# Optimization experiments

Hardware: AMD Instinct MI355X
Metric: run time of the kernel (lower is better)

The kernel has to match this reference:

```python
import jax, jax.numpy as jnp
import numpy as np

MAX_CACHE_LEN = 4096


def _rotate_half(t):
    d = t.shape[-1] // 2
    return jnp.concatenate([-t[..., d:], t[..., :d]], axis=-1)


def _apply_rope(t, cos, sin):
    # t: (B, S, H, D); cos/sin: (S, D)
    c = cos[None, :, None, :]
    s = sin[None, :, None, :]
    return t * c + _rotate_half(t) * s


def setup_inputs() -> dict:
    key = jax.random.key(0)
    ks = jax.random.split(key, 7)
    B, S, E, D, KVH = 1, 2048, 2048, 64, 8
    sc = 0.02
    x = jax.random.normal(ks[0], (B, S, E), dtype=jnp.float32)
    Wq = jax.random.normal(ks[1], (E, E), dtype=jnp.float32) * sc
    Wk = jax.random.normal(ks[2], (KVH * D, E), dtype=jnp.float32) * sc
    Wv = jax.random.normal(ks[3], (KVH * D, E), dtype=jnp.float32) * sc
    Wo = jax.random.normal(ks[4], (E, E), dtype=jnp.float32) * sc
    # RoPE tables
    pos = jnp.arange(S, dtype=jnp.float32)[:, None]
    inv_freq = 1.0 / (10000.0 ** (jnp.arange(0, D, 2, dtype=jnp.float32) / D))
    ang = pos * inv_freq[None, :]              # (S, D/2)
    ang = jnp.concatenate([ang, ang], axis=-1)  # (S, D)
    cos = jnp.cos(ang)
    sin = jnp.sin(ang)
    # additive causal mask (1,1,S,S): 0 where allowed, -1e9 where masked
    causal = jnp.tril(jnp.ones((S, S), dtype=bool))
    attn_mask = jnp.where(causal, 0.0, -1e9).astype(jnp.float32)[None, None]
    return {"x": x, "Wq": Wq, "Wk": Wk, "Wv": Wv, "Wo": Wo,
            "cos": cos, "sin": sin, "attn_mask": attn_mask, "last_pos": S}


def reference(x, Wq, Wk, Wv, Wo, cos, sin, attn_mask, last_pos):
    B, S, E = x.shape
    D = cos.shape[-1]
    H = E // D
    KVH = Wk.shape[0] // D
    group = H // KVH

    q = (x @ Wq.T).reshape(B, S, H, D)
    k = (x @ Wk.T).reshape(B, S, KVH, D)
    v = (x @ Wv.T).reshape(B, S, KVH, D)

    q = _apply_rope(q, cos, sin)
    k = _apply_rope(k, cos, sin)

    # KV-cache write (index_copy at positions [last_pos-S, last_pos)), then slice [:last_pos]
    key_cache = jnp.zeros((B, MAX_CACHE_LEN, KVH, D), dtype=x.dtype)
    value_cache = jnp.zeros((B, MAX_CACHE_LEN, KVH, D), dtype=x.dtype)
    key_cache = jax.lax.dynamic_update_slice(key_cache, jax.lax.stop_gradient(k), (0, last_pos - S, 0, 0))
    value_cache = jax.lax.dynamic_update_slice(value_cache, jax.lax.stop_gradient(v), (0, last_pos - S, 0, 0))
    kc = key_cache[:, :last_pos]    # (B, T, KVH, D)
    vc = value_cache[:, :last_pos]

    # GQA: repeat kv heads to match q heads
    kc = jnp.repeat(kc, group, axis=2)  # (B, T, H, D)
    vc = jnp.repeat(vc, group, axis=2)

    scale = 1.0 / np.sqrt(D)
    scores = jnp.einsum('bqhd,bkhd->bhqk', q, kc) * scale
    scores = scores + attn_mask
    probs = jax.nn.softmax(scores.astype(jnp.float32), axis=-1).astype(x.dtype)
    attn = jnp.einsum('bhqk,bkhd->bqhd', probs, vc)  # (B, S, H, D)
    out = attn.reshape(B, S, E) @ Wo.T
    return out
```

## Files before the change

kernel.cpp:

```cpp
#include <hip/hip_runtime.h>
#include <stdint.h>

typedef unsigned short u16;
typedef unsigned int   u32;

typedef __bf16 bf16x8 __attribute__((ext_vector_type(8)));
typedef float  fx4    __attribute__((ext_vector_type(4)));
typedef u16    u16x8  __attribute__((ext_vector_type(8)));
typedef u16    u16x4  __attribute__((ext_vector_type(4)));

typedef __attribute__((address_space(1))) unsigned int as1_u32;
typedef __attribute__((address_space(3))) unsigned int as3_u32;

__device__ __forceinline__ void gload_lds16(const void* g, void* lds) {
  __builtin_amdgcn_global_load_lds((const as1_u32*)(uintptr_t)g,
                                   (as3_u32*)(uintptr_t)lds, 16, 0, 0);
}

__device__ __forceinline__ float b2f(u32 bits) {
  union { u32 i; float f; } v; v.i = bits << 16; return v.f;
}
__device__ __forceinline__ u16 f2b(float f) {
  union { float f; u32 i; } v; v.f = f;
  u32 x = v.i;
  return (u16)((x + 0x7fffu + ((x >> 16) & 1u)) >> 16);
}
__device__ __forceinline__ u16 f2b_hw(float f) {
  union { __bf16 b; u16 u; } v; v.b = (__bf16)f; return v.u;
}
__device__ __forceinline__ float exp2_hw(float f) {
  return __builtin_amdgcn_exp2f(f);
}

__global__ __launch_bounds__(256) void cast_kernel(
    const float* __restrict__ s0, const float* __restrict__ s1,
    const float* __restrict__ s2, const float* __restrict__ s3,
    const float* __restrict__ s4, u16* __restrict__ dst)
{
  const size_t i8 = ((size_t)blockIdx.x * 256 + threadIdx.x) * 8;
  if (i8 >= 14680064) return;
  const float* src; size_t off;
  if      (i8 <  4194304) { src = s0; off = i8; }
  else if (i8 <  8388608) { src = s1; off = i8 - 4194304; }
  else if (i8 <  9437184) { src = s2; off = i8 - 8388608; }
  else if (i8 < 10485760) { src = s3; off = i8 - 9437184; }
  else                    { src = s4; off = i8 - 10485760; }
  const float4 a = *(const float4*)(src + off);
  const float4 b = *(const float4*)(src + off + 4);
  u16x8 o;
  o[0] = f2b(a.x); o[1] = f2b(a.y); o[2] = f2b(a.z); o[3] = f2b(a.w);
  o[4] = f2b(b.x); o[5] = f2b(b.y); o[6] = f2b(b.z); o[7] = f2b(b.w);
  *(u16x8*)(dst + i8) = o;
}

template <int MODE>
__global__ __launch_bounds__(512) void gemm_bt(
    const u16* __restrict__ A, const u16* __restrict__ B0,
    const u16* __restrict__ B1, const u16* __restrict__ B2,
    void* __restrict__ Cv, int K, int split1, int split2, int ldc,
    const float* __restrict__ cosb, const float* __restrict__ sinb,
    u16* __restrict__ vtg)
{
  __shared__ __align__(16) u16 smem[5 * 8192];

  const int n0 = blockIdx.x * 128;
  const int m0 = blockIdx.y * 128;

  const u16* Bsel; int nb;
  if (n0 < split1)      { Bsel = B0; nb = n0; }
  else if (n0 < split2) { Bsel = B1; nb = n0 - split1; }
  else                  { Bsel = B2; nb = n0 - split2; }

  const int tid  = threadIdx.x;
  const int wave = tid >> 6, lane = tid & 63;
  const int wm = wave >> 1, wn = wave & 1;
  const int quad = lane >> 4, l16 = lane & 15;

  fx4 acc[2][4];
#pragma unroll
  for (int i = 0; i < 2; ++i)
#pragma unroll
    for (int j = 0; j < 4; ++j) acc[i][j] = fx4{0.f, 0.f, 0.f, 0.f};

  const int row = tid >> 2;
  const int ch  = tid & 3;
  const int csw = (ch ^ ((row >> 1) & 3)) * 8;
  auto stage = [&](int kt, int buf) {
    u16* As = smem + buf * 8192;
    u16* Bs = As + 4096;
    const int k0 = kt * 32;
    gload_lds16(A    + (size_t)(m0 + row) * K + k0 + csw, As + tid * 8);
    gload_lds16(Bsel + (size_t)(nb + row) * K + k0 + csw, Bs + tid * 8);
  };

  const int KT = K >> 5;
  stage(0, 0); stage(1, 1); stage(2, 2); stage(3, 3);
  int bufR = 0, bufW = 4;

  const int fx = (l16 >> 1) & 3;
  const int cA = (quad ^ fx) * 8;

#pragma unroll 1
  for (int kt = 0; kt < KT; ++kt) {
    const int rem = KT - 1 - kt;
    if (rem >= 3)      asm volatile("s_waitcnt vmcnt(6)\n\ts_barrier" ::: "memory");
    else if (rem == 2) asm volatile("s_waitcnt vmcnt(4)\n\ts_barrier" ::: "memory");
    else if (rem == 1) asm volatile("s_waitcnt vmcnt(2)\n\ts_barrier" ::: "memory");
    else               asm volatile("s_waitcnt vmcnt(0)\n\ts_barrier" ::: "memory");
    if (kt + 4 < KT) stage(kt + 4, bufW);

    const u16* As = smem + bufR * 8192;
    const u16* Bs = As + 4096;

    bf16x8 af[2], bfr[4];
#pragma unroll
    for (int t = 0; t < 2; ++t)
      af[t]  = *(const bf16x8*)&As[(wm * 32 + t * 16 + l16) * 32 + cA];
#pragma unroll
    for (int t = 0; t < 4; ++t)
      bfr[t] = *(const bf16x8*)&Bs[(wn * 64 + t * 16 + l16) * 32 + cA];
#pragma unroll
    for (int ti = 0; ti < 2; ++ti)
#pragma unroll
      for (int tj = 0; tj < 4; ++tj)
        acc[ti][tj] = __builtin_amdgcn_mfma_f32_16x16x32_bf16(
            af[ti], bfr[tj], acc[ti][tj], 0, 0, 0);

    bufR = (bufR == 4) ? 0 : bufR + 1;
    bufW = (bufW == 4) ? 0 : bufW + 1;
  }

  if (MODE == 1) {
    float* C = (float*)Cv;
#pragma unroll
    for (int ti = 0; ti < 2; ++ti) {
      const int row_b = m0 + wm * 32 + ti * 16 + quad * 4;
#pragma unroll
      for (int tj = 0; tj < 4; ++tj) {
        const int col = n0 + wn * 64 + tj * 16 + l16;
#pragma unroll
        for (int r = 0; r < 4; ++r)
          C[(size_t)(row_b + r) * ldc + col] = acc[ti][tj][r];
      }
    }
  } else {
    u16* C = (u16*)Cv;
    const int cb = n0 + wn * 64;
    if (cb < 2560) {
      const float qs = (cb < 2048) ? 0.18033688f : 1.0f;
#pragma unroll
      for (int ti = 0; ti < 2; ++ti) {
#pragma unroll
        for (int r = 0; r < 4; ++r) {
          const int s = m0 + wm * 32 + ti * 16 + quad * 4 + r;
          const float* cr = cosb + s * 64;
          const float* sr = sinb + s * 64;
          u16* orow = C + (size_t)s * 3072 + cb;
#pragma unroll
          for (int tj = 0; tj < 2; ++tj) {
            const int d0 = tj * 16 + l16, d1 = d0 + 32;
            const float x0 = acc[ti][tj][r], x1 = acc[ti][tj + 2][r];
            orow[d0] = f2b((x0 * cr[d0] - x1 * sr[d0]) * qs);
            orow[d1] = f2b((x1 * cr[d1] + x0 * sr[d1]) * qs);
          }
        }
      }
    } else {
      const int vr0 = cb - 2560;
#pragma unroll
      for (int ti = 0; ti < 2; ++ti) {
        const int s0 = m0 + wm * 32 + ti * 16 + quad * 4;
#pragma unroll
        for (int tj = 0; tj < 4; ++tj) {
          const int vr = vr0 + tj * 16 + l16;
          u16x4 o;
#pragma unroll
          for (int r = 0; r < 4; ++r) o[r] = f2b(acc[ti][tj][r]);
          *(u16x4*)(vtg + (size_t)vr * 2048 + s0) = o;
        }
      }
    }
  }
}

__global__ __launch_bounds__(256) void attn_kernel(
    const u16* __restrict__ qkv, const u16* __restrict__ vt,
    u16* __restrict__ attnbuf)
{
  const int bi  = blockIdx.x;
  const int kvh = bi & 7;
  const int j   = bi >> 3;
  const int h   = kvh * 4 + (j & 3);
  const int bx  = 31 - (j >> 2);
  const int tid = threadIdx.x;
  const int w = tid >> 6, lane = tid & 63;
  const int quad = lane >> 4, l16 = lane & 15;

  __shared__ __align__(16) u16 Qs[64 * 64];
  __shared__ __align__(16) u16 Kb[2][64 * 64];
  __shared__ __align__(16) u16 Vb[2][64 * 64];
  __shared__ __align__(16) u16 Ps[4][16 * 64];

  const int r0    = bx * 64;
  const int nhalf = bx + 1;
  const int kcol  = 2048 + kvh * 64;

  const int srow = tid >> 3;
  const int sc   = tid & 7;

  auto stageQ = [&]() {
#pragma unroll
    for (int i = 0; i < 2; ++i) {
      const int r  = srow + i * 32;
      const int cs = sc ^ (r & 7);
      gload_lds16(qkv + (size_t)(r0 + r) * 3072 + h * 64 + cs * 8,
                  Qs + (size_t)(tid + i * 256) * 8);
    }
  };
  auto stageKV = [&](int n) {
    const int k0 = n * 64;
    u16* Kd = Kb[n & 1];
    u16* Vd = Vb[n & 1];
#pragma unroll
    for (int i = 0; i < 2; ++i) {
      const int r  = srow + i * 32;
      const int cs = sc ^ (r & 7);
      gload_lds16(qkv + (size_t)(k0 + r) * 3072 + kcol + cs * 8,
                  Kd + (size_t)(tid + i * 256) * 8);
      gload_lds16(vt + (size_t)(kvh * 64 + r) * 2048 + k0 + cs * 8,
                  Vd + (size_t)(tid + i * 256) * 8);
    }
  };

  stageQ();
  stageKV(0);
  asm volatile("s_waitcnt vmcnt(0)\n\ts_barrier" ::: "memory");

  const int xm = l16 & 7;
  const int qrow = w * 16 + l16;
  const bf16x8 aq0 = *(const bf16x8*)&Qs[qrow * 64 + ((quad    ) ^ xm) * 8];
  const bf16x8 aq1 = *(const bf16x8*)&Qs[qrow * 64 + ((4 + quad) ^ xm) * 8];

  fx4 O[4];
  float l_r[4];
#pragma unroll
  for (int c = 0; c < 4; ++c) O[c] = fx4{0.f, 0.f, 0.f, 0.f};
#pragma unroll
  for (int r = 0; r < 4; ++r) l_r[r] = 0.f;

#pragma unroll 1
  for (int n = 0; n < nhalf; ++n) {
    if (n + 1 < nhalf) stageKV(n + 1);
    const u16* Kh = Kb[n & 1];
    const u16* Vd = Vb[n & 1];
    const int k0h = n * 64;

    fx4 sc4[4];
    __builtin_amdgcn_s_setprio(1);
#pragma unroll
    for (int c = 0; c < 4; ++c) {
      const int kr = c * 16 + l16;
      const bf16x8 b0 = *(const bf16x8*)&Kh[kr * 64 + ((quad    ) ^ xm) * 8];
      const bf16x8 b1 = *(const bf16x8*)&Kh[kr * 64 + ((4 + quad) ^ xm) * 8];
      fx4 z = fx4{0.f, 0.f, 0.f, 0.f};
      z      = __builtin_amdgcn_mfma_f32_16x16x32_bf16(aq0, b0, z, 0, 0, 0);
      sc4[c] = __builtin_amdgcn_mfma_f32_16x16x32_bf16(aq1, b1, z, 0, 0, 0);
    }
    __builtin_amdgcn_s_setprio(0);

    if (k0h >= r0) {
#pragma unroll
      for (int c = 0; c < 4; ++c)
#pragma unroll
        for (int r = 0; r < 4; ++r) {
          float p = exp2_hw(sc4[c][r]);
          if (k0h + c * 16 + l16 > r0 + w * 16 + quad * 4 + r) p = 0.f;
          l_r[r] += p;
          const int pr = quad * 4 + r;
          Ps[w][pr * 64 + ((c * 16 + l16) ^ ((pr & 7) << 3))] = f2b_hw(p);
        }
    } else {
#pragma unroll
      for (int c = 0; c < 4; ++c)
#pragma unroll
        for (int r = 0; r < 4; ++r) {
          const float p = exp2_hw(sc4[c][r]);
          l_r[r] += p;
          const int pr = quad * 4 + r;
          Ps[w][pr * 64 + ((c * 16 + l16) ^ ((pr & 7) << 3))] = f2b_hw(p);
        }
    }

    const bf16x8 ap0 = *(const bf16x8*)&Ps[w][l16 * 64 + ((quad    ) ^ xm) * 8];
    const bf16x8 ap1 = *(const bf16x8*)&Ps[w][l16 * 64 + ((4 + quad) ^ xm) * 8];
    __builtin_amdgcn_s_setprio(1);
#pragma unroll
    for (int c = 0; c < 4; ++c) {
      const int vr = c * 16 + l16;
      const bf16x8 v0 = *(const bf16x8*)&Vd[vr * 64 + ((quad    ) ^ xm) * 8];
      const bf16x8 v1 = *(const bf16x8*)&Vd[vr * 64 + ((4 + quad) ^ xm) * 8];
      O[c] = __builtin_amdgcn_mfma_f32_16x16x32_bf16(ap0, v0, O[c], 0, 0, 0);
      O[c] = __builtin_amdgcn_mfma_f32_16x16x32_bf16(ap1, v1, O[c], 0, 0, 0);
    }
    __builtin_amdgcn_s_setprio(0);

    asm volatile("s_waitcnt vmcnt(0)\n\ts_barrier" ::: "memory");
  }

#pragma unroll
  for (int r = 0; r < 4; ++r) {
    float l = l_r[r];
#pragma unroll
    for (int off = 1; off < 16; off <<= 1) l += __shfl_xor(l, off, 64);
    const float inv = 1.f / fmaxf(l, 1e-30f);
    const int qg = r0 + w * 16 + quad * 4 + r;
#pragma unroll
    for (int c = 0; c < 4; ++c)
      attnbuf[(size_t)qg * 2048 + h * 64 + c * 16 + l16] = f2b(O[c][r] * inv);
  }
}

extern "C" void kernel_launch(void* const* d_in, const int* in_sizes, int n_in,
                              void* d_out, int out_size, void* d_ws, size_t ws_size,
                              hipStream_t stream) {
  const float* x    = (const float*)d_in[0];
  const float* Wq   = (const float*)d_in[1];
  const float* Wk   = (const float*)d_in[2];
  const float* Wv   = (const float*)d_in[3];
  const float* Wo   = (const float*)d_in[4];
  const float* cosb = (const float*)d_in[5];
  const float* sinb = (const float*)d_in[6];
  float* out = (float*)d_out;

  u16* ws      = (u16*)d_ws;
  u16* qkv     = ws;
  u16* attnbuf = ws + 6291456;
  u16* xb      = ws + 10485760;
  u16* Wqb     = ws + 14680064;
  u16* Wkb     = ws + 18874368;
  u16* Wvb     = ws + 19922944;
  u16* Wob     = ws + 20971520;
  u16* vtg     = ws + 25165824;

  cast_kernel<<<7168, 256, 0, stream>>>(x, Wq, Wk, Wv, Wo, xb);

  gemm_bt<0><<<dim3(24, 16), 512, 0, stream>>>(
      xb, Wqb, Wkb, Wvb, qkv, 2048, 2048, 2560, 3072, cosb, sinb, vtg);

  attn_kernel<<<1024, 256, 0, stream>>>(qkv, vtg, attnbuf);

  gemm_bt<1><<<dim3(16, 16), 512, 0, stream>>>(
      attnbuf, Wob, Wob, Wob, out, 2048, 1 << 30, 1 << 30, 2048, cosb, sinb, vtg);
}
```

Measured before the change: 216.2 us.

## Double GEMM K-tile to 64 with 4-stage LDS ring and XCD-aware block mapping

The GEMM mainloop now stages 64-wide K tiles (two 16-byte loads per thread per operand) in a 4-buffer LDS ring with 3 tiles in flight, using a new 8-way XOR swizzle. Each barrier now covers twice as many MFMAs, so fewer barriers are paid per unit of work. Blocks are also remapped so that consecutive linear block IDs, which are dealt round-robin across the 8 XCDs, place M-tiles sharing the same B column on one XCD to improve L2 reuse. The cost is twice the LDS footprint (128KB), which may lower occupancy. The remap assumes a fixed grid shape (grid.y of 16 tiles).

```diff
diff --git a/kernel.cpp b/kernel.cpp
--- a/kernel.cpp
+++ b/kernel.cpp
@@ -61,10 +61,12 @@
     const float* __restrict__ cosb, const float* __restrict__ sinb,
     u16* __restrict__ vtg)
 {
-  __shared__ __align__(16) u16 smem[5 * 8192];
-
-  const int n0 = blockIdx.x * 128;
-  const int m0 = blockIdx.y * 128;
+  __shared__ __align__(16) u16 smem[4 * 16384];
+
+  const int lin = (int)(blockIdx.y * gridDim.x + blockIdx.x);
+  const int xcd = lin & 7, jj = lin >> 3;
+  const int n0 = (jj >> 1) * 128;
+  const int m0 = (xcd * 2 + (jj & 1)) * 128;
 
   const u16* Bsel; int nb;
   if (n0 < split1)      { Bsel = B0; nb = n0; }
@@ -82,52 +84,57 @@
 #pragma unroll
     for (int j = 0; j < 4; ++j) acc[i][j] = fx4{0.f, 0.f, 0.f, 0.f};
 
-  const int row = tid >> 2;
-  const int ch  = tid & 3;
-  const int csw = (ch ^ ((row >> 1) & 3)) * 8;
+  const int srow = tid >> 3;
+  const int sch  = tid & 7;
+  const int scs  = (sch ^ (srow & 7)) * 8;
   auto stage = [&](int kt, int buf) {
-    u16* As = smem + buf * 8192;
-    u16* Bs = As + 4096;
-    const int k0 = kt * 32;
-    gload_lds16(A    + (size_t)(m0 + row) * K + k0 + csw, As + tid * 8);
-    gload_lds16(Bsel + (size_t)(nb + row) * K + k0 + csw, Bs + tid * 8);
+    u16* As = smem + buf * 16384;
+    u16* Bs = As + 8192;
+    const int k0 = kt * 64;
+#pragma unroll
+    for (int i = 0; i < 2; ++i) {
+      const int r = srow + i * 64;
+      const int s = tid + i * 512;
+      gload_lds16(A    + (size_t)(m0 + r) * K + k0 + scs, As + s * 8);
+      gload_lds16(Bsel + (size_t)(nb + r) * K + k0 + scs, Bs + s * 8);
+    }
   };
 
-  const int KT = K >> 5;
-  stage(0, 0); stage(1, 1); stage(2, 2); stage(3, 3);
-  int bufR = 0, bufW = 4;
-
-  const int fx = (l16 >> 1) & 3;
-  const int cA = (quad ^ fx) * 8;
+  const int KT = K >> 6;
+  stage(0, 0); stage(1, 1); stage(2, 2);
+
+  const int xm = l16 & 7;
 
 #pragma unroll 1
   for (int kt = 0; kt < KT; ++kt) {
     const int rem = KT - 1 - kt;
-    if (rem >= 3)      asm volatile("s_waitcnt vmcnt(6)\n\ts_barrier" ::: "memory");
-    else if (rem == 2) asm volatile("s_waitcnt vmcnt(4)\n\ts_barrier" ::: "memory");
-    else if (rem == 1) asm volatile("s_waitcnt vmcnt(2)\n\ts_barrier" ::: "memory");
+    if (rem >= 2)      asm volatile("s_waitcnt vmcnt(8)\n\ts_barrier" ::: "memory");
+    else if (rem == 1) asm volatile("s_waitcnt vmcnt(4)\n\ts_barrier" ::: "memory");
     else               asm volatile("s_waitcnt vmcnt(0)\n\ts_barrier" ::: "memory");
-    if (kt + 4 < KT) stage(kt + 4, bufW);
-
-    const u16* As = smem + bufR * 8192;
-    const u16* Bs = As + 4096;
-
-    bf16x8 af[2], bfr[4];
-#pragma unroll
-    for (int t = 0; t < 2; ++t)
-      af[t]  = *(const bf16x8*)&As[(wm * 32 + t * 16 + l16) * 32 + cA];
-#pragma unroll
-    for (int t = 0; t < 4; ++t)
-      bfr[t] = *(const bf16x8*)&Bs[(wn * 64 + t * 16 + l16) * 32 + cA];
-#pragma unroll
-    for (int ti = 0; ti < 2; ++ti)
-#pragma unroll
-      for (int tj = 0; tj < 4; ++tj)
-        acc[ti][tj] = __builtin_amdgcn_mfma_f32_16x16x32_bf16(
-            af[ti], bfr[tj], acc[ti][tj], 0, 0, 0);
-
-    bufR = (bufR == 4) ? 0 : bufR + 1;
-    bufW = (bufW == 4) ? 0 : bufW + 1;
+    if (kt + 3 < KT) stage(kt + 3, (kt + 3) & 3);
+
+    const u16* As = smem + (kt & 3) * 16384;
+    const u16* Bs = As + 8192;
+
+    bf16x8 af[2][2], bfr[4][2];
+#pragma unroll
+    for (int kk = 0; kk < 2; ++kk) {
+      const int co = ((kk * 4 + quad) ^ xm) * 8;
+#pragma unroll
+      for (int t = 0; t < 2; ++t)
+        af[t][kk]  = *(const bf16x8*)&As[(wm * 32 + t * 16 + l16) * 64 + co];
+#pragma unroll
+      for (int t = 0; t < 4; ++t)
+        bfr[t][kk] = *(const bf16x8*)&Bs[(wn * 64 + t * 16 + l16) * 64 + co];
+    }
+#pragma unroll
+    for (int kk = 0; kk < 2; ++kk)
+#pragma unroll
+      for (int ti = 0; ti < 2; ++ti)
+#pragma unroll
+        for (int tj = 0; tj < 4; ++tj)
+          acc[ti][tj] = __builtin_amdgcn_mfma_f32_16x16x32_bf16(
+              af[ti][kk], bfr[tj][kk], acc[ti][tj], 0, 0, 0);
   }
 
   if (MODE == 1) {
```

After: 225.8 us. 1.04x slower.
